# Kernel tuning notes

Hardware: AMD Instinct MI355X
Metric: run time of the kernel (lower is better)

Reference implementation:

```python
import jax, jax.numpy as jnp
import numpy as np

B, N, D, H, L = 4, 1024, 256, 4, 2  # batch, nodes, mem_dim, heads, gcn sublayers
DK = D // H


def setup_inputs() -> dict:
    key = jax.random.key(0)
    ks = jax.random.split(key, 12)
    s = 0.05  # weight scale
    return {
        "gcn_inputs": jax.random.normal(ks[0], (B, N, D), jnp.float32),
        "rel_embs": jax.random.normal(ks[1], (B, N, D), jnp.float32),
        "adj": jax.random.randint(ks[2], (B, N, N), 0, 2, jnp.int32),
        "mask": jnp.zeros((B, 1, N), jnp.int32),  # 0 == valid token in this code's convention
        "W_Q": jax.random.normal(ks[3], (2 * D, D), jnp.float32) * s,
        "b_Q": jnp.zeros((D,), jnp.float32),
        "W_K": jax.random.normal(ks[4], (D, D), jnp.float32) * s,
        "b_K": jnp.zeros((D,), jnp.float32),
        "W_gcn": jax.random.normal(ks[5], (H * L, D, D), jnp.float32) * s,
        "b_gcn": jnp.zeros((H * L, D), jnp.float32),
        "W_out": jax.random.normal(ks[6], (D * H * L, D), jnp.float32) * s,
        "b_out": jnp.zeros((D,), jnp.float32),
    }


def _zscore_attn(scores, m, adj):
    """Faithful port of stdzscore + threshold + weightsoftmax chain.
    scores: [B,H,N,N]; m: bool [B,1,1,N] True=valid; adj: int [B,N,N]."""
    mf = m.astype(scores.dtype)
    # mymean (dim=[-1]): count from mask squeezed over dim -2 -> [B,1], +1e-4
    cnt_mean = mf[:, :, 0, :].sum(-1)[..., None] + 1e-4  # [B,1,1]
    ds = jnp.where(m, scores, 0.0).sum(-1)               # [B,H,N]
    mean = ds / cnt_mean                                  # [B,H,N]
    # mystd (dim=[-1]): count from full mask summed over -1 -> [B,1,1], +1e-4
    cnt_std = mf.sum(-1) + 1e-4                           # [B,1,1]
    sdata = jnp.where(m, (scores - mean[..., None]) ** 2, 0.0).sum(-1)
    std = jnp.sqrt(sdata / cnt_std + 1e-10)               # [B,H,N]
    z = (scores - mean[..., None]) / (std[..., None] + 1e-4)
    z = jnp.where(m, z, 0.0)
    thresh = z < 0
    s2 = jnp.where(thresh, -1e9, z)
    s2 = jnp.where(m, s2, -1e9)
    # weightsoftmax: stable exp, multiply by adjacency, mask, renormalize
    e = jnp.exp(s2 - s2.max(-1, keepdims=True))
    e = e * adj.astype(scores.dtype)[:, None]             # [B,H,N,N]
    e = jnp.where(m, e, 0.0) + 1e-10
    w = e / e.sum(-1, keepdims=True)
    w = jnp.where(m, w, 0.0)
    kill = (~m) | thresh | (adj == 0)[:, None]
    return jnp.where(kill, 0.0, w)


def reference(gcn_inputs, rel_embs, adj, mask, W_Q, b_Q, W_K, b_K, W_gcn, b_gcn, W_out, b_out):
    m = (mask == 0)[:, :, None, :]  # [B,1,1,N] True = valid
    # MultiHeadAttention: q from cat(query, rel), k from query
    q = (jnp.concatenate([gcn_inputs, rel_embs], -1) @ W_Q + b_Q)
    q = q.reshape(B, N, H, DK).transpose(0, 2, 1, 3)      # [B,H,N,DK]
    k = (gcn_inputs @ W_K + b_K).reshape(B, N, H, DK).transpose(0, 2, 1, 3)
    scores = jnp.einsum('bhnd,bhmd->bhnm', q, k)
    p_attn = _zscore_attn(scores, m, adj)                 # [B,H,N,N]
    # MultiGraphConvLayer (dropout = identity at inference)
    head_outs = []
    for i in range(H):
        a = p_attn[:, i]                                  # [B,N,N]
        denom = a.sum(2, keepdims=True) + 1.0             # [B,N,1]
        outputs = gcn_inputs
        layer_outs = []
        for l in range(L):
            idx = i * L + l
            Ax = jnp.einsum('bnm,bmd->bnd', a, outputs)
            # Linear applied to BOTH Ax and outputs (bias added twice, as in source)
            AxW = (Ax @ W_gcn[idx] + b_gcn[idx]) + (outputs @ W_gcn[idx] + b_gcn[idx])
            outputs = jax.nn.relu(AxW / denom)
            layer_outs.append(outputs)
        head_outs.append(jnp.concatenate(layer_outs, -1))  # [B,N,D*L]
    final = jnp.concatenate(head_outs, -1)                 # [B,N,D*L*H]
    return gcn_inputs + final @ W_out + b_out
```

## Files before the change

kernel.cpp:

```cpp
#include <hip/hip_runtime.h>
#include <math.h>

typedef unsigned short u16;
typedef __attribute__((ext_vector_type(8))) short short8;
typedef __attribute__((ext_vector_type(4))) float floatx4;

#define LDS_P 72

__device__ __forceinline__ float bf2f(u16 u) {
  union { unsigned int i; float f; } v; v.i = ((unsigned int)u) << 16; return v.f;
}
__device__ __forceinline__ u16 f2bf(float f) {
  union { float f; unsigned int i; } v; v.f = f;
  unsigned int x = v.i;
  return (u16)((x + 0x7FFFu + ((x >> 16) & 1u)) >> 16);
}

__device__ __forceinline__ void mfma_loop(const u16* __restrict__ A, int lda,
                                          const u16* __restrict__ Bt, int ldb,
                                          int K, u16* As, u16* Bs,
                                          floatx4 acc[2][2], int tid) {
  int lane = tid & 63;
  int wm = ((tid >> 6) & 1) << 5, wn = ((tid >> 6) >> 1) << 5;
  int lr = lane & 15, lq8 = (lane >> 4) << 3;
  int r0 = tid >> 3, c8 = (tid & 7) << 3;

  const u16* pA0 = A + (long long)r0 * lda + c8;
  const u16* pA1 = A + (long long)(r0 + 32) * lda + c8;
  const u16* pB0 = Bt + (long long)r0 * ldb + c8;
  const u16* pB1 = Bt + (long long)(r0 + 32) * ldb + c8;
  float4 pa0 = *reinterpret_cast<const float4*>(pA0);
  float4 pa1 = *reinterpret_cast<const float4*>(pA1);
  float4 pb0 = *reinterpret_cast<const float4*>(pB0);
  float4 pb1 = *reinterpret_cast<const float4*>(pB1);

  for (int k0 = 0; k0 < K; k0 += 64) {
    *reinterpret_cast<float4*>(As + r0 * LDS_P + c8) = pa0;
    *reinterpret_cast<float4*>(As + (r0 + 32) * LDS_P + c8) = pa1;
    *reinterpret_cast<float4*>(Bs + r0 * LDS_P + c8) = pb0;
    *reinterpret_cast<float4*>(Bs + (r0 + 32) * LDS_P + c8) = pb1;
    __syncthreads();
    if (k0 + 64 < K) {
      pa0 = *reinterpret_cast<const float4*>(pA0 + k0 + 64);
      pa1 = *reinterpret_cast<const float4*>(pA1 + k0 + 64);
      pb0 = *reinterpret_cast<const float4*>(pB0 + k0 + 64);
      pb1 = *reinterpret_cast<const float4*>(pB1 + k0 + 64);
    }
#pragma unroll
    for (int kc = 0; kc < 64; kc += 32) {
      short8 a0 = *reinterpret_cast<const short8*>(As + (wm + lr) * LDS_P + kc + lq8);
      short8 a1 = *reinterpret_cast<const short8*>(As + (wm + 16 + lr) * LDS_P + kc + lq8);
      short8 b0 = *reinterpret_cast<const short8*>(Bs + (wn + lr) * LDS_P + kc + lq8);
      short8 b1 = *reinterpret_cast<const short8*>(Bs + (wn + 16 + lr) * LDS_P + kc + lq8);
      acc[0][0] = __builtin_amdgcn_mfma_f32_16x16x32_bf16(a0, b0, acc[0][0], 0, 0, 0);
      acc[0][1] = __builtin_amdgcn_mfma_f32_16x16x32_bf16(a0, b1, acc[0][1], 0, 0, 0);
      acc[1][0] = __builtin_amdgcn_mfma_f32_16x16x32_bf16(a1, b0, acc[1][0], 0, 0, 0);
      acc[1][1] = __builtin_amdgcn_mfma_f32_16x16x32_bf16(a1, b1, acc[1][1], 0, 0, 0);
    }
    __syncthreads();
  }
}

#define EPI_SETUP                                                     \
  int lane = threadIdx.x & 63;                                        \
  int wm = ((threadIdx.x >> 6) & 1) << 5,                             \
      wn = ((threadIdx.x >> 6) >> 1) << 5;                            \
  int lr = lane & 15, lq4 = (lane >> 4) << 2;

__global__ __launch_bounds__(256) void proj2_k(
    const u16* __restrict__ A, const u16* __restrict__ WQT,
    const u16* __restrict__ WKT, const float* __restrict__ b_Q,
    const float* __restrict__ b_K, u16* __restrict__ qbf,
    u16* __restrict__ kbf) {
  __shared__ u16 As[64 * LDS_P], Bs[64 * LDS_P];
  int z = blockIdx.z;
  int m0 = blockIdx.y << 6, n0 = blockIdx.x << 6;
  int K = z ? 256 : 512, ldb = z ? 256 : 512;
  const u16* Bt = z ? WKT : WQT;
  const float* bias = z ? b_K : b_Q;
  u16* C = z ? kbf : qbf;
  floatx4 acc[2][2] = {};
  mfma_loop(A + (long long)m0 * 512, 512, Bt + (long long)n0 * ldb, ldb, K, As, Bs,
            acc, threadIdx.x);
  EPI_SETUP
#pragma unroll
  for (int ti = 0; ti < 2; ++ti)
#pragma unroll
    for (int tj = 0; tj < 2; ++tj)
#pragma unroll
      for (int r = 0; r < 4; ++r) {
        int row = m0 + wm + ti * 16 + lq4 + r;
        int col = n0 + wn + tj * 16 + lr;
        C[(long long)row * 256 + col] = f2bf(acc[ti][tj][r] + bias[col]);
      }
}

__global__ __launch_bounds__(256) void mscore_k(
    const u16* __restrict__ q, const u16* __restrict__ kb,
    u16* __restrict__ sc) {
  __shared__ u16 As[64 * LDS_P], Bs[64 * LDS_P];
  int z = blockIdx.z;
  int b = z & 3, h = z >> 2;
  int m0 = blockIdx.y << 6, n0 = blockIdx.x << 6;
  const u16* Ab = q + b * 262144 + h * 64;
  const u16* Bb = kb + b * 262144 + h * 64;
  floatx4 acc[2][2] = {};
  mfma_loop(Ab + (long long)m0 * 256, 256, Bb + (long long)n0 * 256, 256, 64, As, Bs,
            acc, threadIdx.x);
  u16* Cb = sc + ((long long)z << 20);
  EPI_SETUP
#pragma unroll
  for (int ti = 0; ti < 2; ++ti)
#pragma unroll
    for (int tj = 0; tj < 2; ++tj)
#pragma unroll
      for (int r = 0; r < 4; ++r) {
        int row = m0 + wm + ti * 16 + lq4 + r;
        int col = n0 + wn + tj * 16 + lr;
        Cb[(long long)row * 1024 + col] = f2bf(acc[ti][tj][r]);
      }
}

__device__ __forceinline__ float wred_sum(float v) {
#pragma unroll
  for (int m = 32; m > 0; m >>= 1) v += __shfl_xor(v, m, 64);
  return v;
}
__device__ __forceinline__ void wred_sum2(float& a, float& b) {
#pragma unroll
  for (int m = 32; m > 0; m >>= 1) {
    float ta = __shfl_xor(a, m, 64);
    float tb = __shfl_xor(b, m, 64);
    a += ta; b += tb;
  }
}
__device__ __forceinline__ float wred_max(float v) {
#pragma unroll
  for (int m = 32; m > 0; m >>= 1) v = fmaxf(v, __shfl_xor(v, m, 64));
  return v;
}

__global__ __launch_bounds__(256) void zscore_w(
    const u16* __restrict__ sc, const int* __restrict__ adj,
    const int* __restrict__ mask, u16* __restrict__ wout,
    float* __restrict__ denh) {
  int wv = threadIdx.x >> 6, lane = threadIdx.x & 63;
  int row = (blockIdx.x << 2) + wv;
  int b = row >> 10, n = row & 1023;
  int e0 = lane << 4;
  const int* arow = adj + ((long long)row << 10) + e0;
  const int* mrow = mask + (b << 10) + e0;

  unsigned int vbits = 0, abits = 0;
#pragma unroll
  for (int q = 0; q < 4; ++q) {
    int4 a4 = *reinterpret_cast<const int4*>(arow + (q << 2));
    int4 m4 = *reinterpret_cast<const int4*>(mrow + (q << 2));
    vbits |= (unsigned)(m4.x == 0) << (q * 4);
    vbits |= (unsigned)(m4.y == 0) << (q * 4 + 1);
    vbits |= (unsigned)(m4.z == 0) << (q * 4 + 2);
    vbits |= (unsigned)(m4.w == 0) << (q * 4 + 3);
    abits |= (unsigned)(a4.x != 0) << (q * 4);
    abits |= (unsigned)(a4.y != 0) << (q * 4 + 1);
    abits |= (unsigned)(a4.z != 0) << (q * 4 + 2);
    abits |= (unsigned)(a4.w != 0) << (q * 4 + 3);
  }
  float cnt = wred_sum((float)__popc(vbits));
  float cnteff = cnt + 0.0001f;

  for (int h = 0; h < 4; ++h) {
    int z = (h << 2) + b;
    const u16* srow = sc + ((long long)z << 20) + ((long long)n << 10) + e0;
    float s[16];
#pragma unroll
    for (int q = 0; q < 2; ++q) {
      uint4 u = *reinterpret_cast<const uint4*>(srow + (q << 3));
      unsigned int uu[4] = {u.x, u.y, u.z, u.w};
#pragma unroll
      for (int t = 0; t < 4; ++t) {
        union { unsigned int i; float f; } lo, hi;
        lo.i = uu[t] << 16;
        hi.i = uu[t] & 0xffff0000u;
        s[q * 8 + t * 2] = lo.f;
        s[q * 8 + t * 2 + 1] = hi.f;
      }
    }
    float suml = 0.f, sql = 0.f;
#pragma unroll
    for (int u = 0; u < 16; ++u)
      if ((vbits >> u) & 1) { suml += s[u]; sql += s[u] * s[u]; }
    wred_sum2(suml, sql);
    float mean = suml / cnteff;
    float sdata = sql - 2.f * mean * suml + cnt * mean * mean;
    float stdv = sqrtf(fmaxf(sdata, 0.f) / cnteff + 1e-10f);
    float inv = 1.f / (stdv + 0.0001f);

    float maxl = -1e9f;
#pragma unroll
    for (int u = 0; u < 16; ++u) {
      float zz = (s[u] - mean) * inv;
      int vv = (vbits >> u) & 1;
      zz = vv ? zz : 0.f;
      s[u] = zz;
      if (vv && zz >= 0.f) maxl = fmaxf(maxl, zz);
    }
    float rowmax = wred_max(maxl);

    float e[16], el = 0.f;
#pragma unroll
    for (int u = 0; u < 16; ++u) {
      int vv = (vbits >> u) & 1, aa = (abits >> u) & 1;
      float ev = (vv && aa && (s[u] >= 0.f)) ? expf(s[u] - rowmax) : 0.f;
      e[u] = ev + 1e-10f;
      el += e[u];
    }
    float esum = wred_sum(el);
    float rinv = 1.f / esum;

    float wl = 0.f;
    unsigned int wo[8];
#pragma unroll
    for (int u = 0; u < 16; u += 2) {
      int s0 = ((vbits >> u) & 1) && ((abits >> u) & 1) && (s[u] >= 0.f);
      int s1 = ((vbits >> (u + 1)) & 1) && ((abits >> (u + 1)) & 1) && (s[u + 1] >= 0.f);
      float w0 = s0 ? e[u] * rinv : 0.f;
      float w1 = s1 ? e[u + 1] * rinv : 0.f;
      wl += w0 + w1;
      wo[u >> 1] = (unsigned)f2bf(w0) | ((unsigned)f2bf(w1) << 16);
    }
    float wsum = wred_sum(wl);

    u16* orow = wout + ((size_t)z << 20) + ((size_t)n << 10) + e0;
    reinterpret_cast<uint4*>(orow)[0] = make_uint4(wo[0], wo[1], wo[2], wo[3]);
    reinterpret_cast<uint4*>(orow)[1] = make_uint4(wo[4], wo[5], wo[6], wo[7]);
    if (lane == 0) denh[(z << 10) + n] = wsum + 1.0f;
  }
}

__global__ __launch_bounds__(256) void gcn_k(
    const u16* __restrict__ wght, const u16* __restrict__ srcT, int zmaskB,
    const u16* __restrict__ addsrc, int ldadd, long long sAdd, int hmul,
    const u16* __restrict__ WgT_all, const float* __restrict__ bg_all,
    const float* __restrict__ den, int l,
    u16* __restrict__ obT, u16* __restrict__ fin) {
  __shared__ u16 lds[35328];
  u16* As = lds;
  u16* Bs = lds + 4608;
  u16* Ts = lds;
  u16* Ws = lds + 16896;
  int tid = threadIdx.x;
  int m0 = blockIdx.x << 6;
  int z = blockIdx.y;
  int lane = tid & 63, w = tid >> 6;
  int lr = lane & 15, lq8 = (lane >> 4) << 3, lq4 = (lane >> 4) << 2;

  const u16* Aw = wght + ((long long)z << 20) + (long long)m0 * 1024;
  const u16* Bt = srcT + (long long)(z & zmaskB) * 262144;
  const u16* addb = addsrc + (long long)(z & 3) * sAdd + (z >> 2) * hmul;
  int idx2 = (z >> 2) * 2 + l;
  const u16* Wg = WgT_all + (long long)idx2 * 65536;

  floatx4 acc[4][4] = {};
  for (int k0 = 0; k0 < 1024; k0 += 64) {
#pragma unroll
    for (int j = 0; j < 2; ++j) {
      int id = tid + (j << 8);
      int row = id >> 3, c8 = (id & 7) << 3;
      *reinterpret_cast<float4*>(As + row * 72 + c8) =
          *reinterpret_cast<const float4*>(Aw + (long long)row * 1024 + k0 + c8);
    }
#pragma unroll
    for (int j = 0; j < 8; ++j) {
      int id = tid + (j << 8);
      int row = id >> 3, c8 = (id & 7) << 3;
      *reinterpret_cast<float4*>(Bs + row * 72 + c8) =
          *reinterpret_cast<const float4*>(Bt + (long long)row * 1024 + k0 + c8);
    }
    __syncthreads();
#pragma unroll
    for (int kc = 0; kc < 64; kc += 32) {
      short8 a[4], b[4];
#pragma unroll
      for (int t = 0; t < 4; ++t) {
        a[t] = *reinterpret_cast<const short8*>(As + (t * 16 + lr) * 72 + kc + lq8);
        b[t] = *reinterpret_cast<const short8*>(Bs + ((w << 6) + t * 16 + lr) * 72 + kc + lq8);
      }
#pragma unroll
      for (int ti = 0; ti < 4; ++ti)
#pragma unroll
        for (int tj = 0; tj < 4; ++tj)
          acc[ti][tj] =
              __builtin_amdgcn_mfma_f32_16x16x32_bf16(a[ti], b[tj], acc[ti][tj], 0, 0, 0);
    }
    __syncthreads();
  }
#pragma unroll
  for (int ti = 0; ti < 4; ++ti)
#pragma unroll
    for (int tj = 0; tj < 4; ++tj)
#pragma unroll
      for (int r = 0; r < 4; ++r) {
        int row = ti * 16 + lq4 + r;
        int col = (w << 6) + tj * 16 + lr;
        float v = acc[ti][tj][r] + bf2f(addb[(long long)(m0 + row) * ldadd + col]);
        Ts[row * 264 + col] = f2bf(v);
        acc[ti][tj][r] = 0.f;
      }
  __syncthreads();
  for (int kc0 = 0; kc0 < 256; kc0 += 64) {
#pragma unroll
    for (int j = 0; j < 8; ++j) {
      int id = tid + (j << 8);
      int row = id >> 3, c8 = (id & 7) << 3;
      *reinterpret_cast<float4*>(Ws + row * 72 + c8) =
          *reinterpret_cast<const float4*>(Wg + (long long)row * 256 + kc0 + c8);
    }
    __syncthreads();
#pragma unroll
    for (int kc = 0; kc < 64; kc += 32) {
      short8 a[4], b[4];
#pragma unroll
      for (int t = 0; t < 4; ++t) {
        a[t] = *reinterpret_cast<const short8*>(Ts + (t * 16 + lr) * 264 + kc0 + kc + lq8);
        b[t] = *reinterpret_cast<const short8*>(Ws + ((w << 6) + t * 16 + lr) * 72 + kc + lq8);
      }
#pragma unroll
      for (int ti = 0; ti < 4; ++ti)
#pragma unroll
        for (int tj = 0; tj < 4; ++tj)
          acc[ti][tj] =
              __builtin_amdgcn_mfma_f32_16x16x32_bf16(a[ti], b[tj], acc[ti][tj], 0, 0, 0);
    }
    __syncthreads();
  }
  const float* bb = bg_all + idx2 * 256;
  const float* dn = den + (z << 10);
  long long finbase = (long long)(z & 3) * 2097152 + idx2 * 256;
#pragma unroll
  for (int ti = 0; ti < 4; ++ti) {
    int row = m0 + ti * 16 + lq4;
#pragma unroll
    for (int tj = 0; tj < 4; ++tj) {
      int col = (w << 6) + tj * 16 + lr;
      u16 bv4[4];
#pragma unroll
      for (int r = 0; r < 4; ++r) {
        float v = (acc[ti][tj][r] + 2.f * bb[col]) / dn[row + r];
        v = fmaxf(v, 0.f);
        bv4[r] = f2bf(v);
        fin[finbase + (long long)(row + r) * 2048 + col] = bv4[r];
      }
      if (obT) {
        ushort4 t4 = {bv4[0], bv4[1], bv4[2], bv4[3]};
        *reinterpret_cast<ushort4*>(obT + ((long long)z << 18) +
                                    (long long)col * 1024 + row) = t4;
      }
    }
  }
}

__global__ __launch_bounds__(256) void mfinal_k(
    const u16* __restrict__ fin, const u16* __restrict__ WoT,
    float* __restrict__ out) {
  __shared__ u16 As[64 * LDS_P], Bs[64 * LDS_P];
  int m0 = blockIdx.y << 6, n0 = blockIdx.x << 6;
  int ks = blockIdx.z << 9;
  floatx4 acc[2][2] = {};
  mfma_loop(fin + (long long)m0 * 2048 + ks, 2048, WoT + (long long)n0 * 2048 + ks,
            2048, 512, As, Bs, acc, threadIdx.x);
  EPI_SETUP
#pragma unroll
  for (int ti = 0; ti < 2; ++ti)
#pragma unroll
    for (int tj = 0; tj < 2; ++tj)
#pragma unroll
      for (int r = 0; r < 4; ++r) {
        int row = m0 + wm + ti * 16 + lq4 + r;
        int col = n0 + wn + tj * 16 + lr;
        atomicAdd(out + (long long)row * 256 + col, acc[ti][tj][r]);
      }
}

__global__ __launch_bounds__(256) void prep_k(
    const float* __restrict__ X, const float* __restrict__ R,
    const float* __restrict__ W_Q, const float* __restrict__ W_K,
    const float* __restrict__ W_gcn, const float* __restrict__ W_out,
    const float* __restrict__ b_out,
    u16* __restrict__ A, u16* __restrict__ XT, u16* __restrict__ WQT,
    u16* __restrict__ WKT, u16* __restrict__ WgT, u16* __restrict__ WoT,
    float* __restrict__ out) {
  int bi = blockIdx.x;
  int tid = threadIdx.x;
  if (bi < 560) {
    __shared__ u16 tile[64 * LDS_P];
    const float* S;
    u16* D;
    int I, ti, tj;
    if (bi < 256) {
      int zz = bi >> 6, rem = bi & 63;
      ti = rem >> 2; tj = rem & 3; I = 1024;
      S = X + zz * 262144; D = XT + zz * 262144;
    } else if (bi < 288) {
      int t = bi - 256; ti = t >> 2; tj = t & 3; I = 512;
      S = W_Q; D = WQT;
    } else if (bi < 304) {
      int t = bi - 288; ti = t >> 2; tj = t & 3; I = 256;
      S = W_K; D = WKT;
    } else if (bi < 432) {
      int t = bi - 304; int zz = t >> 4, rem = t & 15;
      ti = rem >> 2; tj = rem & 3; I = 256;
      S = W_gcn + zz * 65536; D = WgT + zz * 65536;
    } else {
      int t = bi - 432; ti = t >> 2; tj = t & 3; I = 2048;
      S = W_out; D = WoT;
    }
    int rr = tid >> 4, cc = (tid & 15) << 2;
#pragma unroll
    for (int q = 0; q < 4; ++q) {
      int r = rr + (q << 4);
      float4 v = *reinterpret_cast<const float4*>(S + (long long)(ti * 64 + r) * 256 +
                                                  tj * 64 + cc);
      ushort4 h = {f2bf(v.x), f2bf(v.y), f2bf(v.z), f2bf(v.w)};
      *reinterpret_cast<ushort4*>(tile + r * LDS_P + cc) = h;
    }
    __syncthreads();
    int jl = tid >> 2, il = (tid & 3) << 4;
    u16 vals[16];
#pragma unroll
    for (int u = 0; u < 16; ++u) vals[u] = tile[(il + u) * LDS_P + jl];
    u16* dp = D + (long long)(tj * 64 + jl) * I + ti * 64 + il;
    reinterpret_cast<uint4*>(dp)[0] = *reinterpret_cast<uint4*>(vals);
    reinterpret_cast<uint4*>(dp)[1] = *reinterpret_cast<uint4*>(vals + 8);
  } else if (bi < 8752) {
    int gid = (bi - 560) * 256 + tid;
    int col = gid & 511, row = gid >> 9;
    float v = (col < 256) ? X[row * 256 + col] : R[row * 256 + col - 256];
    A[gid] = f2bf(v);
  } else {
    int t = (bi - 8752) * 256 + tid;
    int col = (t << 2) & 255;
    float4 x = reinterpret_cast<const float4*>(X)[t];
    float4 b = *reinterpret_cast<const float4*>(b_out + col);
    x.x += b.x; x.y += b.y; x.z += b.z; x.w += b.w;
    reinterpret_cast<float4*>(out)[t] = x;
  }
}

extern "C" void kernel_launch(void* const* d_in, const int* in_sizes, int n_in,
                              void* d_out, int out_size, void* d_ws, size_t ws_size,
                              hipStream_t stream) {
  const float* X = (const float*)d_in[0];
  const float* R = (const float*)d_in[1];
  const int* adj = (const int*)d_in[2];
  const int* mask = (const int*)d_in[3];
  const float* W_Q = (const float*)d_in[4];
  const float* b_Q = (const float*)d_in[5];
  const float* W_K = (const float*)d_in[6];
  const float* b_K = (const float*)d_in[7];
  const float* W_gcn = (const float*)d_in[8];
  const float* b_gcn = (const float*)d_in[9];
  const float* W_out = (const float*)d_in[10];
  const float* b_out = (const float*)d_in[11];
  float* out = (float*)d_out;

  u16* wsu = (u16*)d_ws;
  u16* A_qk = wsu;
  u16* qbf  = A_qk + (2u << 20);
  u16* kbf  = qbf + (1u << 20);
  u16* XT   = kbf + (1u << 20);
  u16* WQT  = XT + (1u << 20);
  u16* WKT  = WQT + (1u << 17);
  u16* WgT  = WKT + (1u << 16);
  u16* WoT  = WgT + (1u << 19);
  u16* obT  = WoT + (1u << 19);
  u16* finb = obT + (4u << 20);
  u16* wght = finb + (8u << 20);
  float* den = (float*)(wght + (16u << 20));
  u16* sc = (u16*)(den + (1 << 14));

  prep_k<<<9776, 256, 0, stream>>>(X, R, W_Q, W_K, W_gcn, W_out, b_out,
                                   A_qk, XT, WQT, WKT, WgT, WoT, out);

  proj2_k<<<dim3(4, 64, 2), 256, 0, stream>>>(A_qk, WQT, WKT, b_Q, b_K, qbf, kbf);

  mscore_k<<<dim3(16, 16, 16), 256, 0, stream>>>(qbf, kbf, sc);
  zscore_w<<<1024, 256, 0, stream>>>(sc, adj, mask, wght, den);

  gcn_k<<<dim3(16, 16), 256, 0, stream>>>(wght, XT, 3, A_qk, 512, 524288LL, 0,
                                          WgT, b_gcn, den, 0, obT, finb);
  gcn_k<<<dim3(16, 16), 256, 0, stream>>>(wght, obT, 15, finb, 2048, 2097152LL, 512,
                                          WgT, b_gcn, den, 1, nullptr, finb);

  mfinal_k<<<dim3(4, 64, 4), 256, 0, stream>>>(finb, WoT, out);
}
```

Baseline: 226.7 us.

## Double-buffer LDS tiles in GEMM loops with register prefetch of next slab

Converts the shared mfma_loop and the gcn_k GEMM phases to double-buffered LDS, so the next K-slab is loaded from global into registers during MFMA compute and stored into the alternate buffer. This removes one barrier per iteration and lets global loads overlap compute. In exchange, LDS use roughly doubles (gcn_k goes to about 105KB) and more registers are held live for the prefetch, which can lower occupancy. The Ts/Ws0 aliasing is kept, with Ws0 placed past the Ts region.

```diff
diff --git a/kernel.cpp b/kernel.cpp
--- a/kernel.cpp
+++ b/kernel.cpp
@@ -29,33 +29,45 @@
   const u16* pA1 = A + (long long)(r0 + 32) * lda + c8;
   const u16* pB0 = Bt + (long long)r0 * ldb + c8;
   const u16* pB1 = Bt + (long long)(r0 + 32) * ldb + c8;
-  float4 pa0 = *reinterpret_cast<const float4*>(pA0);
-  float4 pa1 = *reinterpret_cast<const float4*>(pA1);
-  float4 pb0 = *reinterpret_cast<const float4*>(pB0);
-  float4 pb1 = *reinterpret_cast<const float4*>(pB1);
-
-  for (int k0 = 0; k0 < K; k0 += 64) {
-    *reinterpret_cast<float4*>(As + r0 * LDS_P + c8) = pa0;
-    *reinterpret_cast<float4*>(As + (r0 + 32) * LDS_P + c8) = pa1;
-    *reinterpret_cast<float4*>(Bs + r0 * LDS_P + c8) = pb0;
-    *reinterpret_cast<float4*>(Bs + (r0 + 32) * LDS_P + c8) = pb1;
-    __syncthreads();
-    if (k0 + 64 < K) {
-      pa0 = *reinterpret_cast<const float4*>(pA0 + k0 + 64);
-      pa1 = *reinterpret_cast<const float4*>(pA1 + k0 + 64);
-      pb0 = *reinterpret_cast<const float4*>(pB0 + k0 + 64);
-      pb1 = *reinterpret_cast<const float4*>(pB1 + k0 + 64);
+  float4 a0 = *reinterpret_cast<const float4*>(pA0);
+  float4 a1 = *reinterpret_cast<const float4*>(pA1);
+  float4 b0 = *reinterpret_cast<const float4*>(pB0);
+  float4 b1 = *reinterpret_cast<const float4*>(pB1);
+  *reinterpret_cast<float4*>(As + r0 * LDS_P + c8) = a0;
+  *reinterpret_cast<float4*>(As + (r0 + 32) * LDS_P + c8) = a1;
+  *reinterpret_cast<float4*>(Bs + r0 * LDS_P + c8) = b0;
+  *reinterpret_cast<float4*>(Bs + (r0 + 32) * LDS_P + c8) = b1;
+  __syncthreads();
+
+  int nslab = K >> 6;
+  for (int s = 0; s < nslab; ++s) {
+    const u16* Ac = As + (s & 1) * 4608;
+    const u16* Bc = Bs + (s & 1) * 4608;
+    if (s + 1 < nslab) {
+      int off = (s + 1) << 6;
+      a0 = *reinterpret_cast<const float4*>(pA0 + off);
+      a1 = *reinterpret_cast<const float4*>(pA1 + off);
+      b0 = *reinterpret_cast<const float4*>(pB0 + off);
+      b1 = *reinterpret_cast<const float4*>(pB1 + off);
     }
 #pragma unroll
     for (int kc = 0; kc < 64; kc += 32) {
-      short8 a0 = *reinterpret_cast<const short8*>(As + (wm + lr) * LDS_P + kc + lq8);
-      short8 a1 = *reinterpret_cast<const short8*>(As + (wm + 16 + lr) * LDS_P + kc + lq8);
-      short8 b0 = *reinterpret_cast<const short8*>(Bs + (wn + lr) * LDS_P + kc + lq8);
-      short8 b1 = *reinterpret_cast<const short8*>(Bs + (wn + 16 + lr) * LDS_P + kc + lq8);
-      acc[0][0] = __builtin_amdgcn_mfma_f32_16x16x32_bf16(a0, b0, acc[0][0], 0, 0, 0);
-      acc[0][1] = __builtin_amdgcn_mfma_f32_16x16x32_bf16(a0, b1, acc[0][1], 0, 0, 0);
-      acc[1][0] = __builtin_amdgcn_mfma_f32_16x16x32_bf16(a1, b0, acc[1][0], 0, 0, 0);
-      acc[1][1] = __builtin_amdgcn_mfma_f32_16x16x32_bf16(a1, b1, acc[1][1], 0, 0, 0);
+      short8 fa0 = *reinterpret_cast<const short8*>(Ac + (wm + lr) * LDS_P + kc + lq8);
+      short8 fa1 = *reinterpret_cast<const short8*>(Ac + (wm + 16 + lr) * LDS_P + kc + lq8);
+      short8 fb0 = *reinterpret_cast<const short8*>(Bc + (wn + lr) * LDS_P + kc + lq8);
+      short8 fb1 = *reinterpret_cast<const short8*>(Bc + (wn + 16 + lr) * LDS_P + kc + lq8);
+      acc[0][0] = __builtin_amdgcn_mfma_f32_16x16x32_bf16(fa0, fb0, acc[0][0], 0, 0, 0);
+      acc[0][1] = __builtin_amdgcn_mfma_f32_16x16x32_bf16(fa0, fb1, acc[0][1], 0, 0, 0);
+      acc[1][0] = __builtin_amdgcn_mfma_f32_16x16x32_bf16(fa1, fb0, acc[1][0], 0, 0, 0);
+      acc[1][1] = __builtin_amdgcn_mfma_f32_16x16x32_bf16(fa1, fb1, acc[1][1], 0, 0, 0);
+    }
+    if (s + 1 < nslab) {
+      u16* An = As + ((s + 1) & 1) * 4608;
+      u16* Bn = Bs + ((s + 1) & 1) * 4608;
+      *reinterpret_cast<float4*>(An + r0 * LDS_P + c8) = a0;
+      *reinterpret_cast<float4*>(An + (r0 + 32) * LDS_P + c8) = a1;
+      *reinterpret_cast<float4*>(Bn + r0 * LDS_P + c8) = b0;
+      *reinterpret_cast<float4*>(Bn + (r0 + 32) * LDS_P + c8) = b1;
     }
     __syncthreads();
   }
@@ -72,7 +84,7 @@
     const u16* __restrict__ WKT, const float* __restrict__ b_Q,
     const float* __restrict__ b_K, u16* __restrict__ qbf,
     u16* __restrict__ kbf) {
-  __shared__ u16 As[64 * LDS_P], Bs[64 * LDS_P];
+  __shared__ u16 As[2 * 64 * LDS_P], Bs[2 * 64 * LDS_P];
   int z = blockIdx.z;
   int m0 = blockIdx.y << 6, n0 = blockIdx.x << 6;
   int K = z ? 256 : 512, ldb = z ? 256 : 512;
@@ -98,7 +110,7 @@
 __global__ __launch_bounds__(256) void mscore_k(
     const u16* __restrict__ q, const u16* __restrict__ kb,
     u16* __restrict__ sc) {
-  __shared__ u16 As[64 * LDS_P], Bs[64 * LDS_P];
+  __shared__ u16 As[2 * 64 * LDS_P], Bs[2 * 64 * LDS_P];
   int z = blockIdx.z;
   int b = z & 3, h = z >> 2;
   int m0 = blockIdx.y << 6, n0 = blockIdx.x << 6;
@@ -243,11 +255,14 @@
     const u16* __restrict__ WgT_all, const float* __restrict__ bg_all,
     const float* __restrict__ den, int l,
     u16* __restrict__ obT, u16* __restrict__ fin) {
-  __shared__ u16 lds[35328];
-  u16* As = lds;
-  u16* Bs = lds + 4608;
+  __shared__ u16 lds[53760];
+  u16* As0 = lds;
+  u16* As1 = lds + 4608;
+  u16* Bs0 = lds + 9216;
+  u16* Bs1 = lds + 27648;
   u16* Ts = lds;
-  u16* Ws = lds + 16896;
+  u16* Ws0 = lds + 16896;
+  u16* Ws1 = lds + 35328;
   int tid = threadIdx.x;
   int m0 = blockIdx.x << 6;
   int z = blockIdx.y;
@@ -261,29 +276,52 @@
   const u16* Wg = WgT_all + (long long)idx2 * 65536;
 
   floatx4 acc[4][4] = {};
-  for (int k0 = 0; k0 < 1024; k0 += 64) {
-#pragma unroll
-    for (int j = 0; j < 2; ++j) {
-      int id = tid + (j << 8);
-      int row = id >> 3, c8 = (id & 7) << 3;
-      *reinterpret_cast<float4*>(As + row * 72 + c8) =
-          *reinterpret_cast<const float4*>(Aw + (long long)row * 1024 + k0 + c8);
-    }
-#pragma unroll
-    for (int j = 0; j < 8; ++j) {
-      int id = tid + (j << 8);
-      int row = id >> 3, c8 = (id & 7) << 3;
-      *reinterpret_cast<float4*>(Bs + row * 72 + c8) =
-          *reinterpret_cast<const float4*>(Bt + (long long)row * 1024 + k0 + c8);
-    }
-    __syncthreads();
+  float4 pa[2], pb[8];
+  int rowA[2], colA[2], rowB[8], colB[8];
+#pragma unroll
+  for (int j = 0; j < 2; ++j) {
+    int id = tid + (j << 8);
+    rowA[j] = id >> 3; colA[j] = (id & 7) << 3;
+  }
+#pragma unroll
+  for (int j = 0; j < 8; ++j) {
+    int id = tid + (j << 8);
+    rowB[j] = id >> 3; colB[j] = (id & 7) << 3;
+  }
+
+#pragma unroll
+  for (int j = 0; j < 2; ++j)
+    pa[j] = *reinterpret_cast<const float4*>(Aw + (long long)rowA[j] * 1024 + colA[j]);
+#pragma unroll
+  for (int j = 0; j < 8; ++j)
+    pb[j] = *reinterpret_cast<const float4*>(Bt + (long long)rowB[j] * 1024 + colB[j]);
+#pragma unroll
+  for (int j = 0; j < 2; ++j)
+    *reinterpret_cast<float4*>(As0 + rowA[j] * 72 + colA[j]) = pa[j];
+#pragma unroll
+  for (int j = 0; j < 8; ++j)
+    *reinterpret_cast<float4*>(Bs0 + rowB[j] * 72 + colB[j]) = pb[j];
+  __syncthreads();
+
+  for (int s = 0; s < 16; ++s) {
+    const u16* Ac = (s & 1) ? As1 : As0;
+    const u16* Bc = (s & 1) ? Bs1 : Bs0;
+    if (s < 15) {
+      int off = (s + 1) << 6;
+#pragma unroll
+      for (int j = 0; j < 2; ++j)
+        pa[j] = *reinterpret_cast<const float4*>(Aw + (long long)rowA[j] * 1024 + off + colA[j]);
+#pragma unroll
+      for (int j = 0; j < 8; ++j)
+        pb[j] = *reinterpret_cast<const float4*>(Bt + (long long)rowB[j] * 1024 + off + colB[j]);
+    }
 #pragma unroll
     for (int kc = 0; kc < 64; kc += 32) {
       short8 a[4], b[4];
 #pragma unroll
       for (int t = 0; t < 4; ++t) {
-        a[t] = *reinterpret_cast<const short8*>(As + (t * 16 + lr) * 72 + kc + lq8);
-        b[t] = *reinterpret_cast<const short8*>(Bs + ((w << 6) + t * 16 + lr) * 72 + kc + lq8);
+        a[t] = *reinterpret_cast<const short8*>(Ac + (t * 16 + lr) * 72 + kc + lq8);
+        b[t] = *reinterpret_cast<const short8*>(Bc + ((w << 6) + t * 16 + lr) * 72 + kc + lq8);
       }
 #pragma unroll
       for (int ti = 0; ti < 4; ++ti)
@@ -292,8 +330,19 @@
           acc[ti][tj] =
               __builtin_amdgcn_mfma_f32_16x16x32_bf16(a[ti], b[tj], acc[ti][tj], 0, 0, 0);
     }
+    if (s < 15) {
+      u16* An = (s & 1) ? As0 : As1;
+      u16* Bn = (s & 1) ? Bs0 : Bs1;
+#pragma unroll
+      for (int j = 0; j < 2; ++j)
+        *reinterpret_cast<float4*>(An + rowA[j] * 72 + colA[j]) = pa[j];
+#pragma unroll
+      for (int j = 0; j < 8; ++j)
+        *reinterpret_cast<float4*>(Bn + rowB[j] * 72 + colB[j]) = pb[j];
+    }
     __syncthreads();
   }
+
 #pragma unroll
   for (int ti = 0; ti < 4; ++ti)
 #pragma unroll
@@ -306,23 +355,31 @@
         Ts[row * 264 + col] = f2bf(v);
         acc[ti][tj][r] = 0.f;
       }
+  float4 pw[8];
+#pragma unroll
+  for (int j = 0; j < 8; ++j)
+    pw[j] = *reinterpret_cast<const float4*>(Wg + (long long)rowB[j] * 256 + colB[j]);
+#pragma unroll
+  for (int j = 0; j < 8; ++j)
+    *reinterpret_cast<float4*>(Ws0 + rowB[j] * 72 + colB[j]) = pw[j];
   __syncthreads();
-  for (int kc0 = 0; kc0 < 256; kc0 += 64) {
-#pragma unroll
-    for (int j = 0; j < 8; ++j) {
-      int id = tid + (j << 8);
-      int row = id >> 3, c8 = (id & 7) << 3;
-      *reinterpret_cast<float4*>(Ws + row * 72 + c8) =
-          *reinterpret_cast<const float4*>(Wg + (long long)row * 256 + kc0 + c8);
-    }
-    __syncthreads();
+
+  for (int s = 0; s < 4; ++s) {
+    const u16* Wc = (s & 1) ? Ws1 : Ws0;
+    int kc0 = s << 6;
+    if (s < 3) {
+      int off = (s + 1) << 6;
+#pragma unroll
+      for (int j = 0; j < 8; ++j)
+        pw[j] = *reinterpret_cast<const float4*>(Wg + (long long)rowB[j] * 256 + off + colB[j]);
+    }
 #pragma unroll
     for (int kc = 0; kc < 64; kc += 32) {
       short8 a[4], b[4];
 #pragma unroll
       for (int t = 0; t < 4; ++t) {
         a[t] = *reinterpret_cast<const short8*>(Ts + (t * 16 + lr) * 264 + kc0 + kc + lq8);
-        b[t] = *reinterpret_cast<const short8*>(Ws + ((w << 6) + t * 16 + lr) * 72 + kc + lq8);
+        b[t] = *reinterpret_cast<const short8*>(Wc + ((w << 6) + t * 16 + lr) * 72 + kc + lq8);
       }
 #pragma unroll
       for (int ti = 0; ti < 4; ++ti)
@@ -331,8 +388,15 @@
           acc[ti][tj] =
               __builtin_amdgcn_mfma_f32_16x16x32_bf16(a[ti], b[tj], acc[ti][tj], 0, 0, 0);
     }
+    if (s < 3) {
+      u16* Wn = (s & 1) ? Ws0 : Ws1;
+#pragma unroll
+      for (int j = 0; j < 8; ++j)
+        *reinterpret_cast<float4*>(Wn + rowB[j] * 72 + colB[j]) = pw[j];
+    }
     __syncthreads();
   }
+
   const float* bb = bg_all + idx2 * 256;
   const float* dn = den + (z << 10);
   long long finbase = (long long)(z & 3) * 2097152 + idx2 * 256;
@@ -362,7 +426,7 @@
 __global__ __launch_bounds__(256) void mfinal_k(
     const u16* __restrict__ fin, const u16* __restrict__ WoT,
     float* __restrict__ out) {
-  __shared__ u16 As[64 * LDS_P], Bs[64 * LDS_P];
+  __shared__ u16 As[2 * 64 * LDS_P], Bs[2 * 64 * LDS_P];
   int m0 = blockIdx.y << 6, n0 = blockIdx.x << 6;
   int ks = blockIdx.z << 9;
   floatx4 acc[2][2] = {};
```

Measured after the change: 227.3 us. Within noise of the previous version (+0.2%).
